# Kernel optimization log

Measured on AMD Instinct MI355X. Metric: run time of the kernel, lower is better.

Reference implementation:

```python
import jax, jax.numpy as jnp
import numpy as np

N = 50000      # nodes
E = 1600000    # edges
IN_DIM = 128
HID = 32
OUT = 32
HEADS = 4
NEG_SLOPE = 0.2  # DGL GATConv default leaky_relu slope


def setup_inputs() -> dict:
    key = jax.random.key(0)
    ks = jax.random.split(key, 16)
    h = jax.random.normal(ks[0], (N, IN_DIM), dtype=jnp.float32)
    src = jax.random.randint(ks[1], (E,), 0, N, dtype=jnp.int32)
    dst = jax.random.randint(ks[2], (E,), 0, N, dtype=jnp.int32)
    s = 0.1
    # layer 1: in_dim -> (HEADS, HID)
    W1 = jax.random.normal(ks[3], (IN_DIM, HEADS * HID), dtype=jnp.float32) * s
    al1 = jax.random.normal(ks[4], (HEADS, HID), dtype=jnp.float32) * s
    ar1 = jax.random.normal(ks[5], (HEADS, HID), dtype=jnp.float32) * s
    b1 = jnp.zeros((HEADS * HID,), dtype=jnp.float32)
    # layer 2: HEADS*HID -> (HEADS, HID)
    W2 = jax.random.normal(ks[6], (HEADS * HID, HEADS * HID), dtype=jnp.float32) * s
    al2 = jax.random.normal(ks[7], (HEADS, HID), dtype=jnp.float32) * s
    ar2 = jax.random.normal(ks[8], (HEADS, HID), dtype=jnp.float32) * s
    b2 = jnp.zeros((HEADS * HID,), dtype=jnp.float32)
    # layer 3: HEADS*HID -> (HEADS, OUT)
    W3 = jax.random.normal(ks[9], (HEADS * HID, HEADS * OUT), dtype=jnp.float32) * s
    al3 = jax.random.normal(ks[10], (HEADS, OUT), dtype=jnp.float32) * s
    ar3 = jax.random.normal(ks[11], (HEADS, OUT), dtype=jnp.float32) * s
    b3 = jnp.zeros((HEADS * OUT,), dtype=jnp.float32)
    return {"h": h, "src": src, "dst": dst,
            "W1": W1, "al1": al1, "ar1": ar1, "b1": b1,
            "W2": W2, "al2": al2, "ar2": ar2, "b2": b2,
            "W3": W3, "al3": al3, "ar3": ar3, "b3": b3}


def gat_layer(h, W, al, ar, b, src, dst):
    """DGL-style GATConv. h:[N,F] -> [N,H,D]."""
    H, D = al.shape
    ft = (h @ W).reshape(-1, H, D)                      # [N,H,D]
    el = jnp.einsum('nhd,hd->nh', ft, al)               # [N,H]
    er = jnp.einsum('nhd,hd->nh', ft, ar)               # [N,H]
    e = jax.nn.leaky_relu(el[src] + er[dst], NEG_SLOPE)  # [E,H]
    # edge softmax grouped by destination node
    m = jax.ops.segment_max(e, dst, num_segments=N)     # [N,H]
    ex = jnp.exp(e - m[dst])
    z = jax.ops.segment_sum(ex, dst, num_segments=N)    # [N,H]
    a = ex / z[dst]                                     # [E,H]
    msg = ft[src] * a[:, :, None]                       # [E,H,D]
    rst = jax.ops.segment_sum(msg, dst, num_segments=N)  # [N,H,D]
    return rst + b.reshape(1, H, D)


def reference(h, src, dst, W1, al1, ar1, b1, W2, al2, ar2, b2, W3, al3, ar3, b3):
    x = gat_layer(h, W1, al1, ar1, b1, src, dst).reshape(N, -1)  # flatten(1)
    x = jax.nn.elu(x)  # dropout is identity at eval
    x = gat_layer(x, W2, al2, ar2, b2, src, dst).reshape(N, -1)
    x = jax.nn.elu(x)
    x = gat_layer(x, W3, al3, ar3, b3, src, dst).mean(axis=1)    # [N,OUT]
    return x
```

## Files before the change

kernel.cpp:

```cpp
#include <hip/hip_runtime.h>
#include <hip/hip_fp16.h>

#define NEG_SLOPE 0.2f
#define LOG2E 1.44269504088896340736f
#define C1   2048
#define BKT  196
#define BSTR 9216

typedef _Float16 half8 __attribute__((ext_vector_type(8)));
typedef float    f32x4 __attribute__((ext_vector_type(4)));

__device__ __forceinline__ unsigned int encf(float f) {
    unsigned int u = __float_as_uint(f);
    return (u & 0x80000000u) ? ~u : (u | 0x80000000u);
}
__device__ __forceinline__ float decf(unsigned int u) {
    return (u & 0x80000000u) ? __uint_as_float(u & 0x7fffffffu)
                             : __uint_as_float(~u);
}


__device__ __forceinline__ void wprep_body(char* SM, int b,
    const float* __restrict__ W1, const float* __restrict__ W2,
    const float* __restrict__ W3, __half* __restrict__ Wt)
{
    float (*tile)[33] = (float(*)[33])SM;
    const float* W = (b < 16) ? W1 : (b < 32) ? W2 : W3;
    __half* out = Wt + (size_t)(b >> 4) * (128 * 128);
    const int tb = b & 15;
    const int k0 = (tb >> 2) * 32;
    const int c0 = (tb & 3) * 32;
    const int t = threadIdx.x;
    const int tx = t & 31, ty = t >> 5;
#pragma unroll
    for (int p = 0; p < 4; ++p)
        tile[p * 8 + ty][tx] = W[(size_t)(k0 + p * 8 + ty) * 128 + c0 + tx];
    __syncthreads();
#pragma unroll
    for (int p = 0; p < 4; ++p) {
        const int c = c0 + p * 8 + ty;
        out[(size_t)c * 128 + k0 + tx] = __float2half(tile[tx][p * 8 + ty]);
    }
}

__device__ __forceinline__ void p1_body(char* SM, int blk,
    const int* __restrict__ src, const int* __restrict__ dst,
    unsigned int* __restrict__ tmp, unsigned int* __restrict__ bcnt, int E_)
{
    unsigned int* hist  = (unsigned int*)SM;
    unsigned int* sc    = hist + 256;
    unsigned int* ebase = sc + 256;
    unsigned int* gbase = ebase + 256;
    unsigned int* buf   = gbase + 256;
    unsigned int* off   = buf + C1;
    const int t  = threadIdx.x;
    const int e0 = blk * C1;
    hist[t] = 0;
    __syncthreads();
    int  s_[8], d_[8];
    bool v_[8];
#pragma unroll
    for (int k = 0; k < 2; ++k) {
        int idx = e0 + k * 1024 + t * 4;
        if (idx + 3 < E_) {
            int4 sv = *(const int4*)&src[idx];
            int4 dv = *(const int4*)&dst[idx];
            s_[k*4+0]=sv.x; s_[k*4+1]=sv.y; s_[k*4+2]=sv.z; s_[k*4+3]=sv.w;
            d_[k*4+0]=dv.x; d_[k*4+1]=dv.y; d_[k*4+2]=dv.z; d_[k*4+3]=dv.w;
            v_[k*4+0]=true; v_[k*4+1]=true; v_[k*4+2]=true; v_[k*4+3]=true;
        } else {
            for (int j = 0; j < 4; ++j) {
                int e = idx + j;
                v_[k*4+j] = e < E_;
                s_[k*4+j] = v_[k*4+j] ? src[e] : 0;
                d_[k*4+j] = v_[k*4+j] ? dst[e] : 0;
            }
        }
    }
#pragma unroll
    for (int j = 0; j < 8; ++j) if (v_[j]) atomicAdd(&hist[d_[j] >> 8], 1u);
    __syncthreads();
    const unsigned int cnt_t = hist[t];
    sc[t] = cnt_t;
    __syncthreads();
    for (int o = 1; o < 256; o <<= 1) {
        unsigned int v = (t >= o) ? sc[t - o] : 0;
        __syncthreads();
        sc[t] += v;
        __syncthreads();
    }
    const unsigned int excl = sc[t] - cnt_t;
    ebase[t] = excl;
    gbase[t] = (t < BKT && cnt_t > 0) ? atomicAdd(&bcnt[t], cnt_t) : 0u;
    hist[t] = excl;
    __syncthreads();
#pragma unroll
    for (int j = 0; j < 8; ++j) {
        if (v_[j]) {
            const int b = d_[j] >> 8;
            unsigned int pos  = atomicAdd(&hist[b], 1u);
            unsigned int go   = gbase[b] + (pos - ebase[b]);
            buf[pos] = ((unsigned int)s_[j] << 8) | (unsigned int)(d_[j] & 255);
            off[pos] = (go < BSTR) ? ((unsigned int)b * BSTR + go) : 0xFFFFFFFFu;
        }
    }
    __syncthreads();
    const int total = min(C1, E_ - e0);
    for (int i = t; i < total; i += 256) {
        unsigned int u = off[i];
        if (u != 0xFFFFFFFFu) tmp[u] = buf[i];
    }
}

__device__ __forceinline__ void p2_body(char* SM, int b,
    const unsigned int* __restrict__ tmp, const unsigned int* __restrict__ bcnt,
    int* __restrict__ rowptr, int* __restrict__ esrc_s, int Nn)
{
    unsigned int* ent  = (unsigned int*)SM;
    unsigned int* hist = ent + BSTR;
    unsigned int* sc   = hist + 256;
    unsigned int* cur  = sc + 256;
    const int t = threadIdx.x;
    const unsigned int vt = (t < BKT) ? bcnt[t] : 0;
    sc[t] = vt;
    __syncthreads();
    for (int o = 1; o < 256; o <<= 1) {
        unsigned int u = (t >= o) ? sc[t - o] : 0;
        __syncthreads();
        sc[t] += u;
        __syncthreads();
    }
    const unsigned int base = (b > 0) ? sc[b - 1] : 0;
    const unsigned int cnt  = min(bcnt[b], (unsigned int)BSTR);
    __syncthreads();
    hist[t] = 0;
    __syncthreads();
    for (unsigned int i = t; i < cnt; i += 256) {
        unsigned int e = tmp[(size_t)b * BSTR + i];
        ent[i] = e;
        atomicAdd(&hist[e & 255u], 1u);
    }
    __syncthreads();
    const unsigned int c_t = hist[t];
    sc[t] = c_t;
    __syncthreads();
    for (int o = 1; o < 256; o <<= 1) {
        unsigned int u = (t >= o) ? sc[t - o] : 0;
        __syncthreads();
        sc[t] += u;
        __syncthreads();
    }
    const unsigned int excl = sc[t] - c_t;
    cur[t] = base + excl;
    const int n = (b << 8) + t;
    if (n <= Nn) rowptr[n] = (int)(base + excl);
    __syncthreads();
    for (unsigned int i = t; i < cnt; i += 256) {
        unsigned int e = ent[i];
        unsigned int p = atomicAdd(&cur[e & 255u], 1u);
        esrc_s[p] = (int)(e >> 8);
    }
}

__device__ __forceinline__ void gemm_body(char* SMEM, unsigned int* lmax,
    int row0, const float* __restrict__ X, const __half* __restrict__ Wt,
    const float* __restrict__ al, const float* __restrict__ ar,
    __half* __restrict__ C16, float* __restrict__ el, float* __restrict__ er,
    unsigned int* __restrict__ maxbuf, int M)
{
    char* Xs = SMEM;
    char* Ws = SMEM + 64 * 256;
    const int t = threadIdx.x;
    const int l = t & 63;
    const int w = t >> 6;
    if (t < 8) lmax[t] = 0;

    {
        const int r = t >> 2;
        int gr = row0 + r; if (gr >= M) gr = M - 1;
        const float4* s4 = (const float4*)&X[(size_t)gr * 128 + (t & 3) * 32];
        const unsigned swz = ((unsigned)(r & 7)) << 4;
        char* base = Xs + r * 256;
#pragma unroll
        for (int u = 0; u < 4; ++u) {
            float4 a = s4[2 * u], b = s4[2 * u + 1];
            half8 hv;
            hv[0] = (_Float16)a.x; hv[1] = (_Float16)a.y;
            hv[2] = (_Float16)a.z; hv[3] = (_Float16)a.w;
            hv[4] = (_Float16)b.x; hv[5] = (_Float16)b.y;
            hv[6] = (_Float16)b.z; hv[7] = (_Float16)b.w;
            *(half8*)(base + (((t & 3) * 64 + u * 16) ^ swz)) = hv;
        }
    }
    {
        const int c = t >> 1;
        const char* src = (const char*)Wt + (size_t)c * 256 + (t & 1) * 128;
        const unsigned swz = ((unsigned)(c & 7)) << 4;
        char* base = Ws + c * 256;
#pragma unroll
        for (int u = 0; u < 8; ++u) {
            uint4 v = *(const uint4*)(src + u * 16);
            *(uint4*)(base + (((t & 1) * 128 + u * 16) ^ swz)) = v;
        }
    }
    __syncthreads();

    const int wr = w * 16;
    const int rA = l & 15;
    const int kq = l >> 4;

    half8 af[4];
    {
        const int row = wr + rA;
        const unsigned swz = ((unsigned)(row & 7)) << 4;
        const char* base = Xs + row * 256;
#pragma unroll
        for (int kk = 0; kk < 4; ++kk)
            af[kk] = *(const half8*)(base + (((unsigned)(kk * 64 + kq * 16)) ^ swz));
    }
    f32x4 acc[8];
#pragma unroll
    for (int ct = 0; ct < 8; ++ct) { acc[ct][0]=0.f; acc[ct][1]=0.f; acc[ct][2]=0.f; acc[ct][3]=0.f; }
#pragma unroll
    for (int ct = 0; ct < 8; ++ct) {
        const int c = ct * 16 + rA;
        const unsigned swz = ((unsigned)(c & 7)) << 4;
        const char* base = Ws + c * 256;
#pragma unroll
        for (int kk = 0; kk < 4; ++kk) {
            half8 bf = *(const half8*)(base + (((unsigned)(kk * 64 + kq * 16)) ^ swz));
            acc[ct] = __builtin_amdgcn_mfma_f32_16x16x32_f16(af[kk], bf, acc[ct], 0, 0, 0);
        }
    }

    float pl[4][4], pr[4][4];
#pragma unroll
    for (int h = 0; h < 4; ++h)
#pragma unroll
        for (int r = 0; r < 4; ++r) { pl[h][r] = 0.f; pr[h][r] = 0.f; }
#pragma unroll
    for (int ct = 0; ct < 8; ++ct) {
        const int col = ct * 16 + rA;
        const float av = al[col] * LOG2E;
        const float rv = ar[col] * LOG2E;
        const int h = ct >> 1;
#pragma unroll
        for (int r = 0; r < 4; ++r) {
            pl[h][r] += acc[ct][r] * av;
            pr[h][r] += acc[ct][r] * rv;
        }
    }
#pragma unroll
    for (int off = 1; off < 16; off <<= 1) {
#pragma unroll
        for (int h = 0; h < 4; ++h)
#pragma unroll
            for (int r = 0; r < 4; ++r) {
                pl[h][r] += __shfl_xor(pl[h][r], off);
                pr[h][r] += __shfl_xor(pr[h][r], off);
            }
    }
    if (rA == 0) {
#pragma unroll
        for (int r = 0; r < 4; ++r) {
            const int gr = row0 + wr + kq * 4 + r;
            if (gr < M) {
                *(float4*)&el[(size_t)gr * 4] =
                    make_float4(pl[0][r], pl[1][r], pl[2][r], pl[3][r]);
                *(float4*)&er[(size_t)gr * 4] =
                    make_float4(pr[0][r], pr[1][r], pr[2][r], pr[3][r]);
            }
        }
#pragma unroll
        for (int h = 0; h < 4; ++h) {
            float ml = fmaxf(fmaxf(pl[h][0], pl[h][1]), fmaxf(pl[h][2], pl[h][3]));
            float mr = fmaxf(fmaxf(pr[h][0], pr[h][1]), fmaxf(pr[h][2], pr[h][3]));
            atomicMax(&lmax[h], encf(ml));
            atomicMax(&lmax[4 + h], encf(mr));
        }
    }

    {
        char* slice = Xs + wr * 256;
#pragma unroll
        for (int ct = 0; ct < 8; ++ct) {
            const int colb = (ct * 16 + rA) * 2;
#pragma unroll
            for (int r = 0; r < 4; ++r) {
                const int rowL = kq * 4 + r;
                const unsigned swz = ((unsigned)(rowL & 7)) << 4;
                *(__half*)(slice + rowL * 256 + ((unsigned)colb ^ swz)) =
                    __float2half(acc[ct][r]);
            }
        }
        const int rowL = l >> 2;
        const unsigned swz = ((unsigned)(rowL & 7)) << 4;
        const int gr = row0 + wr + rowL;
#pragma unroll
        for (int u = 0; u < 4; ++u) {
            const unsigned bo = (unsigned)((l & 3) * 64 + u * 16);
            uint4 v = *(const uint4*)(slice + rowL * 256 + (bo ^ swz));
            if (gr < M) *(uint4*)&C16[(size_t)gr * 128 + bo / 2] = v;
        }
    }
    __syncthreads();
    if (t < 8) atomicMax(&maxbuf[t], lmax[t]);
}


__global__ __launch_bounds__(256) void fusedA(const float* __restrict__ W1,
    const float* __restrict__ W2, const float* __restrict__ W3,
    __half* __restrict__ Wt, const int* __restrict__ src,
    const int* __restrict__ dst, unsigned int* __restrict__ tmp,
    unsigned int* __restrict__ bcnt, int E_)
{
    __shared__ __align__(16) char SM[20480];
    if (blockIdx.x < 48) wprep_body(SM, blockIdx.x, W1, W2, W3, Wt);
    else                 p1_body(SM, blockIdx.x - 48, src, dst, tmp, bcnt, E_);
}

__global__ __launch_bounds__(256) void fusedB(const float* __restrict__ X,
    const __half* __restrict__ Wt, const float* __restrict__ al,
    const float* __restrict__ ar, __half* __restrict__ C16,
    float* __restrict__ el, float* __restrict__ er,
    unsigned int* __restrict__ maxbuf, int M, int MG,
    const unsigned int* __restrict__ tmp, const unsigned int* __restrict__ bcnt,
    int* __restrict__ rowptr, int* __restrict__ esrc_s)
{
    __shared__ __align__(16) char SMEM[49152];
    __shared__ unsigned int lmax[8];
    if ((int)blockIdx.x < MG)
        gemm_body(SMEM, lmax, blockIdx.x * 64, X, Wt, al, ar, C16, el, er, maxbuf, M);
    else
        p2_body(SMEM, blockIdx.x - MG, tmp, bcnt, rowptr, esrc_s, M);
}

__global__ __launch_bounds__(256) void gemm_mfma(const float* __restrict__ X,
    const __half* __restrict__ Wt, const float* __restrict__ al,
    const float* __restrict__ ar, __half* __restrict__ C16,
    float* __restrict__ el, float* __restrict__ er,
    unsigned int* __restrict__ maxbuf, int M)
{
    __shared__ __align__(16) char SMEM[49152];
    __shared__ unsigned int lmax[8];
    gemm_body(SMEM, lmax, blockIdx.x * 64, X, Wt, al, ar, C16, el, er, maxbuf, M);
}

template <int MODE>
__global__ __launch_bounds__(256) void attn_agg(
    const __half* __restrict__ ft, const float* __restrict__ el,
    const float* __restrict__ er, const int* __restrict__ rowptr,
    const int* __restrict__ esrc, const float* __restrict__ bias,
    const unsigned int* __restrict__ mbuf, float* __restrict__ out, int Nn)
{
    const int t = threadIdx.x;
    const int l = t & 63;
    const int n = blockIdx.x * 4 + (t >> 6);
    if (n >= Nn) return;
    const int g    = l >> 4;
    const int q    = l & 15;
    const int head = q >> 2;

    const int start = rowptr[n];
    const int end   = rowptr[n + 1];
    const bool any  = end > start;

    const float er_h = er[(size_t)n * 4 + head];
    const float msum = decf(mbuf[head]) + decf(mbuf[4 + head]);
    const float mh   = msum > 0.f ? msum : NEG_SLOPE * msum;

    const char* __restrict__ ftb = (const char*)ft;
    const char* __restrict__ elb = (const char*)el;
    const unsigned qo = (unsigned)q << 4;
    const unsigned ho = (unsigned)head << 2;

    float acc[8];
#pragma unroll
    for (int j = 0; j < 8; ++j) acc[j] = 0.f;
    float z = 0.f;

    const int c0   = start & ~3;
    const int last = end - 1;
    const int span = end - start;

    int  sA = 0, sB = 0, sC = 0;
    uint4 fA = make_uint4(0,0,0,0), fB;
    float eA = 0.f, eB;

    if (any) {
        int e0i = min(max(c0 + g, start), last);
        int e1i = min(max(c0 + 4 + g, start), last);
        sA = esrc[e0i];
        sB = esrc[e1i];
        fA = *(const uint4*)(ftb + ((unsigned)sA << 8) + qo);
        eA = *(const float*)(elb + ((unsigned)sA << 4) + ho);
    }

#pragma unroll 2
    for (int c = c0; c < end; c += 4) {
        sC = esrc[min(c + 8 + g, last)];
        fB = *(const uint4*)(ftb + ((unsigned)sB << 8) + qo);
        eB = *(const float*)(elb + ((unsigned)sB << 4) + ho);
        {
            const int e = c + g;
            float x = eA + er_h;
            x = fmaxf(x, NEG_SLOPE * x);
            float ex = __builtin_amdgcn_exp2f(x - mh);
            ex = ((unsigned)(e - start) < (unsigned)span) ? ex : 0.f;
            z += ex;
            const half8 hv = __builtin_bit_cast(half8, fA);
            acc[0] += (float)hv[0] * ex;
            acc[1] += (float)hv[1] * ex;
            acc[2] += (float)hv[2] * ex;
            acc[3] += (float)hv[3] * ex;
            acc[4] += (float)hv[4] * ex;
            acc[5] += (float)hv[5] * ex;
            acc[6] += (float)hv[6] * ex;
            acc[7] += (float)hv[7] * ex;
        }
        sA = sB; sB = sC; fA = fB; eA = eB;
    }

#pragma unroll
    for (int j = 0; j < 8; ++j) {
        acc[j] += __shfl_xor(acc[j], 16);
        acc[j] += __shfl_xor(acc[j], 32);
    }
    z += __shfl_xor(z, 16);
    z += __shfl_xor(z, 32);

    const float inv = any ? 1.f / z : 0.f;

    if (MODE == 0) {
        if (l < 32) {
            float r0, r1, r2, r3;
            if (l < 16) { r0 = acc[0]; r1 = acc[1]; r2 = acc[2]; r3 = acc[3]; }
            else        { r0 = acc[4]; r1 = acc[5]; r2 = acc[6]; r3 = acc[7]; }
            const int f0 = 8 * q + 4 * (l >> 4);
            const float4 b4 = *(const float4*)&bias[f0];
            float vx = r0 * inv + b4.x;
            float vy = r1 * inv + b4.y;
            float vz = r2 * inv + b4.z;
            float vw = r3 * inv + b4.w;
            vx = vx > 0.f ? vx : __expf(vx) - 1.f;
            vy = vy > 0.f ? vy : __expf(vy) - 1.f;
            vz = vz > 0.f ? vz : __expf(vz) - 1.f;
            vw = vw > 0.f ? vw : __expf(vw) - 1.f;
            *(float4*)&out[(size_t)n * 128 + f0] = make_float4(vx, vy, vz, vw);
        }
    } else {
        float v[8];
        const float4 ba = *(const float4*)&bias[8 * q];
        const float4 bb = *(const float4*)&bias[8 * q + 4];
        v[0] = acc[0] * inv + ba.x; v[1] = acc[1] * inv + ba.y;
        v[2] = acc[2] * inv + ba.z; v[3] = acc[3] * inv + ba.w;
        v[4] = acc[4] * inv + bb.x; v[5] = acc[5] * inv + bb.y;
        v[6] = acc[6] * inv + bb.z; v[7] = acc[7] * inv + bb.w;
#pragma unroll
        for (int j = 0; j < 8; ++j) {
            v[j] += __shfl_xor(v[j], 4);
            v[j] += __shfl_xor(v[j], 8);
        }
        if (l < 4) {
            *(float4*)&out[(size_t)n * 32 + 8 * q] =
                make_float4(0.25f * v[0], 0.25f * v[1], 0.25f * v[2], 0.25f * v[3]);
            *(float4*)&out[(size_t)n * 32 + 8 * q + 4] =
                make_float4(0.25f * v[4], 0.25f * v[5], 0.25f * v[6], 0.25f * v[7]);
        }
    }
}

extern "C" void kernel_launch(void* const* d_in, const int* in_sizes, int n_in,
                              void* d_out, int out_size, void* d_ws, size_t ws_size,
                              hipStream_t stream)
{
    const float* h   = (const float*)d_in[0];
    const int*   src = (const int*)d_in[1];
    const int*   dst = (const int*)d_in[2];
    const float* W1  = (const float*)d_in[3];
    const float* al1 = (const float*)d_in[4];
    const float* ar1 = (const float*)d_in[5];
    const float* b1  = (const float*)d_in[6];
    const float* W2  = (const float*)d_in[7];
    const float* al2 = (const float*)d_in[8];
    const float* ar2 = (const float*)d_in[9];
    const float* b2  = (const float*)d_in[10];
    const float* W3  = (const float*)d_in[11];
    const float* al3 = (const float*)d_in[12];
    const float* ar3 = (const float*)d_in[13];
    const float* b3  = (const float*)d_in[14];

    const int N = in_sizes[0] / 128;
    const int E = in_sizes[1];

    char* p = (char*)d_ws;
    auto alloc = [&](size_t bytes) {
        void* r = (void*)p;
        p += (bytes + 255) & ~(size_t)255;
        return r;
    };
    __half* ft    = (__half*)alloc((size_t)N * 128 * 2);
    float* xA     = (float*)alloc((size_t)N * 128 * 4);
    float* elbuf  = (float*)alloc((size_t)N * 4 * 4);
    float* erbuf  = (float*)alloc((size_t)N * 4 * 4);
    int*   rowptr = (int*)alloc((size_t)(N + 1) * 4);
    int*   esrc_s = (int*)alloc((size_t)E * 4);
    unsigned int* bcnt   = (unsigned int*)alloc((256 + 24) * 4);
    unsigned int* maxbuf = bcnt + 256;
    __half* Wt    = (__half*)alloc((size_t)3 * 128 * 128 * 2);

    unsigned int* tmp = (unsigned int*)xA;

    const int NG4 = (N + 3) / 4;
    const int MG  = (N + 63) / 64;
    const int G1  = (E + C1 - 1) / C1;

    hipMemsetAsync(bcnt, 0, (256 + 24) * 4, stream);
    fusedA<<<48 + G1, 256, 0, stream>>>(W1, W2, W3, Wt, src, dst, tmp, bcnt, E);
    fusedB<<<MG + BKT, 256, 0, stream>>>(h, Wt, al1, ar1, ft, elbuf, erbuf,
                                         maxbuf, N, MG, tmp, bcnt, rowptr, esrc_s);
    attn_agg<0><<<NG4, 256, 0, stream>>>(ft, elbuf, erbuf, rowptr, esrc_s, b1, maxbuf, xA, N);

    gemm_mfma<<<MG, 256, 0, stream>>>(xA, Wt + 128 * 128, al2, ar2, ft, elbuf, erbuf, maxbuf + 8, N);
    attn_agg<0><<<NG4, 256, 0, stream>>>(ft, elbuf, erbuf, rowptr, esrc_s, b2, maxbuf + 8, xA, N);

    gemm_mfma<<<MG, 256, 0, stream>>>(xA, Wt + 2 * 128 * 128, al3, ar3, ft, elbuf, erbuf, maxbuf + 16, N);
    attn_agg<1><<<NG4, 256, 0, stream>>>(ft, elbuf, erbuf, rowptr, esrc_s, b3, maxbuf + 16,
                                         (float*)d_out, N);
}
```

Baseline: 374.2 us.

## Deepen gather prefetch, read GEMM weights directly, and double edge-bucketing chunk size

The attention aggregation loop now prefetches two edges ahead instead of one, to hide more gather latency on ft/el rows. The GEMM no longer stages the transposed weights into shared memory and reads B fragments straight from global (L2-cached) memory, which cuts LDS use and a barrier-bound copy. The edge partitioning pass handles 4096 edges per block instead of 2048, halving block count but raising LDS and register use. Direct global weight loads may raise latency per MFMA, and the larger chunk may lower occupancy.

```diff
diff --git a/kernel.cpp b/kernel.cpp
--- a/kernel.cpp
+++ b/kernel.cpp
@@ -3,7 +3,7 @@
 
 #define NEG_SLOPE 0.2f
 #define LOG2E 1.44269504088896340736f
-#define C1   2048
+#define C1   4096
 #define BKT  196
 #define BSTR 9216
 
@@ -57,10 +57,10 @@
     const int e0 = blk * C1;
     hist[t] = 0;
     __syncthreads();
-    int  s_[8], d_[8];
-    bool v_[8];
-#pragma unroll
-    for (int k = 0; k < 2; ++k) {
+    int  s_[16], d_[16];
+    bool v_[16];
+#pragma unroll
+    for (int k = 0; k < 4; ++k) {
         int idx = e0 + k * 1024 + t * 4;
         if (idx + 3 < E_) {
             int4 sv = *(const int4*)&src[idx];
@@ -78,7 +78,7 @@
         }
     }
 #pragma unroll
-    for (int j = 0; j < 8; ++j) if (v_[j]) atomicAdd(&hist[d_[j] >> 8], 1u);
+    for (int j = 0; j < 16; ++j) if (v_[j]) atomicAdd(&hist[d_[j] >> 8], 1u);
     __syncthreads();
     const unsigned int cnt_t = hist[t];
     sc[t] = cnt_t;
@@ -95,7 +95,7 @@
     hist[t] = excl;
     __syncthreads();
 #pragma unroll
-    for (int j = 0; j < 8; ++j) {
+    for (int j = 0; j < 16; ++j) {
         if (v_[j]) {
             const int b = d_[j] >> 8;
             unsigned int pos  = atomicAdd(&hist[b], 1u);
@@ -169,7 +169,6 @@
     unsigned int* __restrict__ maxbuf, int M)
 {
     char* Xs = SMEM;
-    char* Ws = SMEM + 64 * 256;
     const int t = threadIdx.x;
     const int l = t & 63;
     const int w = t >> 6;
@@ -192,17 +191,6 @@
             *(half8*)(base + (((t & 3) * 64 + u * 16) ^ swz)) = hv;
         }
     }
-    {
-        const int c = t >> 1;
-        const char* src = (const char*)Wt + (size_t)c * 256 + (t & 1) * 128;
-        const unsigned swz = ((unsigned)(c & 7)) << 4;
-        char* base = Ws + c * 256;
-#pragma unroll
-        for (int u = 0; u < 8; ++u) {
-            uint4 v = *(const uint4*)(src + u * 16);
-            *(uint4*)(base + (((t & 1) * 128 + u * 16) ^ swz)) = v;
-        }
-    }
     __syncthreads();
 
     const int wr = w * 16;
@@ -218,19 +206,21 @@
         for (int kk = 0; kk < 4; ++kk)
             af[kk] = *(const half8*)(base + (((unsigned)(kk * 64 + kq * 16)) ^ swz));
     }
+    const char* wb = (const char*)Wt + (unsigned)rA * 256 + (unsigned)kq * 16;
     f32x4 acc[8];
 #pragma unroll
     for (int ct = 0; ct < 8; ++ct) { acc[ct][0]=0.f; acc[ct][1]=0.f; acc[ct][2]=0.f; acc[ct][3]=0.f; }
 #pragma unroll
     for (int ct = 0; ct < 8; ++ct) {
-        const int c = ct * 16 + rA;
-        const unsigned swz = ((unsigned)(c & 7)) << 4;
-        const char* base = Ws + c * 256;
-#pragma unroll
-        for (int kk = 0; kk < 4; ++kk) {
-            half8 bf = *(const half8*)(base + (((unsigned)(kk * 64 + kq * 16)) ^ swz));
-            acc[ct] = __builtin_amdgcn_mfma_f32_16x16x32_f16(af[kk], bf, acc[ct], 0, 0, 0);
-        }
+        const char* base = wb + (unsigned)(ct * 16) * 256;
+        half8 bf0 = *(const half8*)(base);
+        half8 bf1 = *(const half8*)(base + 64);
+        half8 bf2 = *(const half8*)(base + 128);
+        half8 bf3 = *(const half8*)(base + 192);
+        acc[ct] = __builtin_amdgcn_mfma_f32_16x16x32_f16(af[0], bf0, acc[ct], 0, 0, 0);
+        acc[ct] = __builtin_amdgcn_mfma_f32_16x16x32_f16(af[1], bf1, acc[ct], 0, 0, 0);
+        acc[ct] = __builtin_amdgcn_mfma_f32_16x16x32_f16(af[2], bf2, acc[ct], 0, 0, 0);
+        acc[ct] = __builtin_amdgcn_mfma_f32_16x16x32_f16(af[3], bf3, acc[ct], 0, 0, 0);
     }
 
     float pl[4][4], pr[4][4];
@@ -314,7 +304,7 @@
     const int* __restrict__ dst, unsigned int* __restrict__ tmp,
     unsigned int* __restrict__ bcnt, int E_)
 {
-    __shared__ __align__(16) char SM[20480];
+    __shared__ __align__(16) char SM[36864];
     if (blockIdx.x < 48) wprep_body(SM, blockIdx.x, W1, W2, W3, Wt);
     else                 p1_body(SM, blockIdx.x - 48, src, dst, tmp, bcnt, E_);
 }
@@ -327,7 +317,7 @@
     const unsigned int* __restrict__ tmp, const unsigned int* __restrict__ bcnt,
     int* __restrict__ rowptr, int* __restrict__ esrc_s)
 {
-    __shared__ __align__(16) char SMEM[49152];
+    __shared__ __align__(16) char SMEM[39936];
     __shared__ unsigned int lmax[8];
     if ((int)blockIdx.x < MG)
         gemm_body(SMEM, lmax, blockIdx.x * 64, X, Wt, al, ar, C16, el, er, maxbuf, M);
@@ -341,7 +331,7 @@
     float* __restrict__ el, float* __restrict__ er,
     unsigned int* __restrict__ maxbuf, int M)
 {
-    __shared__ __align__(16) char SMEM[49152];
+    __shared__ __align__(16) char SMEM[16384];
     __shared__ unsigned int lmax[8];
     gemm_body(SMEM, lmax, blockIdx.x * 64, X, Wt, al, ar, C16, el, er, maxbuf, M);
 }
@@ -383,24 +373,28 @@
     const int last = end - 1;
     const int span = end - start;
 
-    int  sA = 0, sB = 0, sC = 0;
-    uint4 fA = make_uint4(0,0,0,0), fB;
-    float eA = 0.f, eB;
+    int  sA = 0, sB = 0, sC = 0, sD = 0;
+    uint4 fA = make_uint4(0,0,0,0), fB = fA, fC;
+    float eA = 0.f, eB = 0.f, eC;
 
     if (any) {
         int e0i = min(max(c0 + g, start), last);
         int e1i = min(max(c0 + 4 + g, start), last);
+        int e2i = min(max(c0 + 8 + g, start), last);
         sA = esrc[e0i];
         sB = esrc[e1i];
+        sC = esrc[e2i];
         fA = *(const uint4*)(ftb + ((unsigned)sA << 8) + qo);
         eA = *(const float*)(elb + ((unsigned)sA << 4) + ho);
-    }
-
-#pragma unroll 2
-    for (int c = c0; c < end; c += 4) {
-        sC = esrc[min(c + 8 + g, last)];
         fB = *(const uint4*)(ftb + ((unsigned)sB << 8) + qo);
         eB = *(const float*)(elb + ((unsigned)sB << 4) + ho);
+    }
+
+#pragma unroll 3
+    for (int c = c0; c < end; c += 4) {
+        sD = esrc[min(c + 12 + g, last)];
+        fC = *(const uint4*)(ftb + ((unsigned)sC << 8) + qo);
+        eC = *(const float*)(elb + ((unsigned)sC << 4) + ho);
         {
             const int e = c + g;
             float x = eA + er_h;
@@ -418,7 +412,9 @@
             acc[6] += (float)hv[6] * ex;
             acc[7] += (float)hv[7] * ex;
         }
-        sA = sB; sB = sC; fA = fB; eA = eB;
+        sA = sB; sB = sC; sC = sD;
+        fA = fB; fB = fC;
+        eA = eB; eB = eC;
     }
 
 #pragma unroll
```

New measurement: 375.8 us. About the same (+0.4%).
